# Kernel tuning notes

Measured on AMD Instinct MI355X. Metric: run time of the kernel, lower is better.

Reference implementation:

```python
import jax, jax.numpy as jnp
import numpy as np

# GNB per-element parameters [s, beta, R, C6] indexed by atomic number Z (rows not listed stay zero)
_ROWS = {
 1:[0.2772,1.7504,3.6516,95.99], 2:[0.2425,2.087,2.1843,40.67], 3:[0.3266,2.3073,1.2711,70.21],
 4:[0.3964,2.8811,3.3497,114.51], 5:[0.3121,2.6366,2.7079,152.36], 6:[0.2455,3.0189,1.8219,184.28],
 7:[0.2743,2.9432,2.4667,482.54], 8:[0.2577,2.7407,2.365,405.57], 9:[0.2791,2.5863,1.5062,218.45],
 10:[0.2378,2.5307,1.8233,174.81], 11:[0.2592,2.5679,1.3974,181.7], 12:[0.3837,2.9613,3.3515,263.02],
 13:[0.3013,3.2377,3.0102,228.1], 14:[0.3202,3.2749,3.1629,359.43], 15:[0.3399,3.7491,3.2554,3222.12],
 16:[0.3215,3.6718,2.9539,2144.49], 17:[0.3071,3.418,3.0368,2072.46], 18:[0.2752,3.3306,2.6598,1357.42],
 19:[0.2264,2.9736,4.0877,1406.65], 20:[0.4015,3.4464,4.1275,1058.36], 21:[0.9388,4.5955,9.7282,11498.73],
 22:[0.6048,3.5334,8.5322,3361.33], 23:[0.3678,3.068,7.2344,2095.91], 24:[0.2848,2.8393,5.3605,1049.31],
 25:[0.355,3.055,3.718,966.27], 26:[0.4406,3.2628,3.6408,1571.36], 27:[0.4124,3.2622,3.4961,1183.59],
 28:[0.3139,2.749,3.5108,787.76], 29:[0.3345,2.9097,3.0537,563.93], 30:[0.3391,2.9024,3.0261,592.91],
 31:[0.3146,3.3924,3.1735,430.82], 32:[0.3327,3.2804,3.1773,812.57], 33:[0.404,3.8757,3.8357,4533.53],
 34:[0.3343,3.8562,3.1109,3440.92], 35:[0.3242,3.7067,3.2122,3859.82], 36:[0.292,3.6457,2.8263,2729.6],
 37:[0.2677,3.4421,2.412,1864.19], 38:[0.3446,3.559,1.894,1175.73], 39:[1.0038,5.7293,11.2061,32141.18],
 40:[0.6146,5.075,6.821,27655.14], 41:[0.4244,3.7156,7.2367,2864.2], 42:[0.4882,3.6853,3.901,3563.45],
 43:[0.4439,3.6987,4.0857,3266.43], 44:[0.4736,3.7826,4.045,3967.23], 45:[0.4039,3.4706,3.4813,2233.82],
 46:[0.3188,3.3433,3.0487,1393.49], 47:[0.2948,3.1186,2.7795,1315.09], 48:[0.3012,3.0853,2.8673,1311.47],
 49:[0.3351,3.5452,3.3339,1460.56], 50:[0.3134,3.2997,3.0086,1662.99], 51:[0.4081,4.1277,3.9919,8089.97],
 52:[0.3585,4.1795,3.4209,6887.05], 53:[0.3574,4.0988,3.5649,8799.32], 54:[0.3134,4.0387,3.0288,6136.5],
 55:[0.2872,3.8468,2.262,3757.31], 56:[0.3788,4.0368,1.3837,2561.18], 57:[1.0851,6.1365,12.171,66580.83],
 72:[0.5577,5.213,6.0791,27593.76], 73:[0.5308,4.7637,5.7661,15364.65], 74:[0.3926,3.6018,3.6366,2734.5],
 75:[0.5351,3.9552,4.241,4801.82], 76:[0.4701,4.0278,4.1348,5685.94], 77:[0.3661,3.6123,3.4213,2786.0],
 78:[0.3411,3.6066,3.2486,2699.79], 79:[0.3164,3.3822,2.9588,2282.6], 80:[0.3047,3.375,2.9381,2476.79],
 81:[0.2802,3.3964,2.7711,2988.7], 82:[0.2682,3.2481,2.5816,2506.63], 83:[0.3876,4.1225,3.785,8916.84],
 84:[0.3679,4.2313,3.5381,8694.22], 85:[0.368,4.2455,3.6985,11821.61], 86:[0.3195,4.1784,3.0551,8410.64],
}
_TAB = np.zeros((87, 4), np.float32)
for _z, _v in _ROWS.items():
    _TAB[_z] = _v
GNB_TABLE = jnp.asarray(_TAB)
C_SP2 = jnp.asarray(np.array([0.2808, 3.0548, 2.2348, 429.69], np.float32))
C_SP3 = jnp.asarray(np.array([0.2455, 3.0189, 1.8219, 184.28], np.float32))
N_CN2 = jnp.asarray(np.array([0.2996, 3.02, 2.6454, 720.18], np.float32))
N_CN3 = jnp.asarray(np.array([0.2743, 2.9432, 2.4667, 482.54], np.float32))

BJ_A1, BJ_A2, BJ_ALPHA = 0.4, 4.0, 14.0
CUTOFF_LR, CUTOFF_START = 10.0, 8.0  # cutoff_start = cutoff_lr - 2.0


def _poly_envelope(x):
    # PolynomialCutoff.calculate_envelope with r_max=1, p=6:
    x6 = x ** 6
    env = 1.0 - 28.0 * x6 + 48.0 * x6 * x - 21.0 * x6 * x * x
    return env * (x < 1.0)


def _gnb_forward(lengths, Z, edge_index):
    n_nodes = Z.shape[0]
    sender, receiver = edge_index[0], edge_index[1]

    # coordination numbers via scatter-add on receiver
    cn = jnp.zeros((n_nodes,), jnp.int32).at[receiver].add(1)

    # species-indexed params with CN-adaptive selection for C and N
    params = GNB_TABLE[Z]  # [N, 4]
    c_params = jnp.where((cn <= 3)[:, None], C_SP2[None, :], C_SP3[None, :])
    n_params = jnp.where((cn <= 2)[:, None], N_CN2[None, :], N_CN3[None, :])
    params = jnp.where((Z == 6)[:, None], c_params, params)
    params = jnp.where((Z == 7)[:, None], n_params, params)

    R_i = params[:, 2]
    C6_i = params[:, 3]

    # geometric-mean combination rules per edge
    C6_ij = jnp.sqrt(C6_i[sender] * C6_i[receiver])
    R_ij = jnp.sqrt(R_i[sender] * R_i[receiver])

    r = lengths
    # BJ damping: f = 1 / (1 + 6 (r/r0)^(-alpha)), r0 = a1 sqrt(R_ij) + a2
    r0 = BJ_A1 * jnp.sqrt(R_ij) + BJ_A2
    f_damp = 1.0 / (1.0 + 6.0 * (r0 / r) ** BJ_ALPHA)

    e_edge = -C6_ij / (R_ij ** 6 + r ** 6) * f_damp

    # long-range polynomial cutoff switching from 1 at cutoff_start to 0 at cutoff_lr
    x = (r - CUTOFF_START) / (CUTOFF_LR - CUTOFF_START)
    env = jnp.where(r < CUTOFF_START, 1.0, _poly_envelope(x))
    e_edge = e_edge * env

    # scatter-sum to atoms; 0.5 to split symmetric pair energy over both directions
    node_energy = jnp.zeros((n_nodes,), e_edge.dtype).at[receiver].add(0.5 * e_edge)
    return node_energy


def setup_inputs() -> dict:
    key = jax.random.key(0)
    k1, k2, k3 = jax.random.split(key, 3)
    n_nodes, n_edges = 100000, 6400000
    Z = jax.random.randint(k1, (n_nodes,), 1, 87, dtype=jnp.int32)
    edge_index = jax.random.randint(k2, (2, n_edges), 0, n_nodes, dtype=jnp.int32)
    lengths = jax.random.uniform(k3, (n_edges,), jnp.float32, 1.0, 10.5)
    return {"Z": Z, "edge_index": edge_index, "lengths": lengths}


def reference(Z, edge_index, lengths):
    return _gnb_forward(lengths, Z, edge_index)
```

## Files before the change

### kernel.cpp

```cpp
#include <hip/hip_runtime.h>


#define B2SHIFT 10
#define B2SIZE  1024
#define TILE    4096
#define ESLICES 16
#define MAXB    128

__device__ __constant__ float2 GNB_RC6[87] = {
    {0.f, 0.f},
    {3.6516f, 95.99f},   {2.1843f, 40.67f},   {1.2711f, 70.21f},
    {3.3497f, 114.51f},  {2.7079f, 152.36f},  {1.8219f, 184.28f},
    {2.4667f, 482.54f},  {2.365f, 405.57f},   {1.5062f, 218.45f},
    {1.8233f, 174.81f},  {1.3974f, 181.7f},   {3.3515f, 263.02f},
    {3.0102f, 228.1f},   {3.1629f, 359.43f},  {3.2554f, 3222.12f},
    {2.9539f, 2144.49f}, {3.0368f, 2072.46f}, {2.6598f, 1357.42f},
    {4.0877f, 1406.65f}, {4.1275f, 1058.36f}, {9.7282f, 11498.73f},
    {8.5322f, 3361.33f}, {7.2344f, 2095.91f}, {5.3605f, 1049.31f},
    {3.718f, 966.27f},   {3.6408f, 1571.36f}, {3.4961f, 1183.59f},
    {3.5108f, 787.76f},  {3.0537f, 563.93f},  {3.0261f, 592.91f},
    {3.1735f, 430.82f},  {3.1773f, 812.57f},  {3.8357f, 4533.53f},
    {3.1109f, 3440.92f}, {3.2122f, 3859.82f}, {2.8263f, 2729.6f},
    {2.412f, 1864.19f},  {1.894f, 1175.73f},  {11.2061f, 32141.18f},
    {6.821f, 27655.14f}, {7.2367f, 2864.2f},  {3.901f, 3563.45f},
    {4.0857f, 3266.43f}, {4.045f, 3967.23f},  {3.4813f, 2233.82f},
    {3.0487f, 1393.49f}, {2.7795f, 1315.09f}, {2.8673f, 1311.47f},
    {3.3339f, 1460.56f}, {3.0086f, 1662.99f}, {3.9919f, 8089.97f},
    {3.4209f, 6887.05f}, {3.5649f, 8799.32f}, {3.0288f, 6136.5f},
    {2.262f, 3757.31f},  {1.3837f, 2561.18f}, {12.171f, 66580.83f},
    {0.f,0.f},{0.f,0.f},{0.f,0.f},{0.f,0.f},{0.f,0.f},{0.f,0.f},{0.f,0.f},
    {0.f,0.f},{0.f,0.f},{0.f,0.f},{0.f,0.f},{0.f,0.f},{0.f,0.f},{0.f,0.f},
    {6.0791f, 27593.76f}, {5.7661f, 15364.65f}, {3.6366f, 2734.5f},
    {4.241f, 4801.82f},   {4.1348f, 5685.94f},  {3.4213f, 2786.0f},
    {3.2486f, 2699.79f},  {2.9588f, 2282.6f},   {2.9381f, 2476.79f},
    {2.7711f, 2988.7f},   {2.5816f, 2506.63f},  {3.785f, 8916.84f},
    {3.5381f, 8694.22f},  {3.6985f, 11821.61f}, {3.0551f, 8410.64f},
};

__global__ void gnb_init(const int* __restrict__ Z, unsigned* __restrict__ isCN,
                         int nw, int n_nodes, int* __restrict__ zp, int zwords) {
    int stride = gridDim.x * blockDim.x;
    int t0 = blockIdx.x * blockDim.x + threadIdx.x;
    for (int i = t0; i < zwords; i += stride) zp[i] = 0;
    for (int w = t0; w < nw; w += stride) {
        unsigned m = 0;
        int base = w << 5;
        int lim = n_nodes - base; if (lim > 32) lim = 32;
        for (int k = 0; k < lim; ++k) {
            int z = Z[base + k];
            if (z == 6 || z == 7) m |= (1u << k);
        }
        isCN[w] = m;
    }
}

__global__ void __launch_bounds__(256)
gnb_scatter(const int* __restrict__ send, const int* __restrict__ recv,
            const float* __restrict__ len, const unsigned* __restrict__ isCN,
            int* __restrict__ cn,
            uint2* __restrict__ buckets, unsigned* __restrict__ cursor,
            uint4* __restrict__ ovrec, unsigned* __restrict__ ocur,
            int n_edges, int cap, unsigned ocap, int NB2) {
    __shared__ unsigned cnt[MAXB];
    __shared__ unsigned pos[MAXB];
    __shared__ unsigned startp[MAXB + 1];
    __shared__ unsigned gbase[MAXB];
    __shared__ uint2 srec[TILE];
    __shared__ unsigned char bmap[TILE];
    const int tid = threadIdx.x;
    const int e0  = blockIdx.x * TILE;

    for (int b = tid; b < MAXB; b += 256) { cnt[b] = 0; pos[b] = 0; }
    __syncthreads();

    #pragma unroll
    for (int k = 0; k < 4; ++k) {
        int base = e0 + (k * 256 + tid) * 4;
        if (base + 3 < n_edges) {
            int4 rv = *(const int4*)(recv + base);
            int rr[4] = {rv.x, rv.y, rv.z, rv.w};
            #pragma unroll
            for (int j = 0; j < 4; ++j) {
                unsigned r = (unsigned)rr[j];
                atomicAdd(&cnt[r >> B2SHIFT], 1u);
                if ((isCN[r >> 5] >> (r & 31)) & 1u) atomicAdd(&cn[r], 1);
            }
        } else {
            int lim = n_edges - base; if (lim > 4) lim = 4;
            for (int j = 0; j < lim; ++j) {
                unsigned r = (unsigned)recv[base + j];
                atomicAdd(&cnt[r >> B2SHIFT], 1u);
                if ((isCN[r >> 5] >> (r & 31)) & 1u) atomicAdd(&cn[r], 1);
            }
        }
    }
    __syncthreads();

    if (tid == 0) {
        unsigned acc = 0;
        for (int b = 0; b < NB2; ++b) { startp[b] = acc; acc += cnt[b]; }
        startp[NB2] = acc;
    }
    __syncthreads();
    if (tid < NB2) gbase[tid] = atomicAdd(&cursor[tid], cnt[tid]);
    __syncthreads();

    #pragma unroll
    for (int k = 0; k < 4; ++k) {
        int base = e0 + (k * 256 + tid) * 4;
        if (base + 3 < n_edges) {
            int4  sv = *(const int4*)(send + base);
            int4  rv = *(const int4*)(recv + base);
            uint4 lv = *(const uint4*)(len + base);
            int ss[4] = {sv.x, sv.y, sv.z, sv.w};
            int rr[4] = {rv.x, rv.y, rv.z, rv.w};
            unsigned ll[4] = {lv.x, lv.y, lv.z, lv.w};
            #pragma unroll
            for (int j = 0; j < 4; ++j) {
                unsigned r = (unsigned)rr[j];
                unsigned b = r >> B2SHIFT;
                unsigned slot = startp[b] + atomicAdd(&pos[b], 1u);
                srec[slot] = make_uint2((unsigned)ss[j] | ((r & (B2SIZE - 1)) << 17), ll[j]);
                bmap[slot] = (unsigned char)b;
            }
        } else {
            int lim = n_edges - base; if (lim > 4) lim = 4;
            for (int j = 0; j < lim; ++j) {
                unsigned r = (unsigned)recv[base + j];
                unsigned b = r >> B2SHIFT;
                unsigned slot = startp[b] + atomicAdd(&pos[b], 1u);
                srec[slot] = make_uint2((unsigned)send[base + j] | ((r & (B2SIZE - 1)) << 17),
                                        ((const unsigned*)len)[base + j]);
                bmap[slot] = (unsigned char)b;
            }
        }
    }
    __syncthreads();

    unsigned total = startp[NB2];
    for (unsigned i = tid; i < total; i += 256) {
        unsigned b = bmap[i];
        unsigned g = gbase[b] + (i - startp[b]);
        uint2 rec = srec[i];
        if (g < (unsigned)cap) {
            buckets[(size_t)b * cap + g] = rec;
        } else {
            unsigned o = atomicAdd(ocur, 1u);
            unsigned r = ((unsigned)b << B2SHIFT) | ((rec.x >> 17) & (B2SIZE - 1));
            if (o < ocap) ovrec[o] = make_uint4(r, rec.x & 0x1FFFFu, rec.y, 0u);
        }
    }
}

__global__ void gnb_params(const int* __restrict__ Z, const int* __restrict__ cn,
                           float2* __restrict__ P2, int n_nodes) {
    int i = blockIdx.x * blockDim.x + threadIdx.x;
    if (i >= n_nodes) return;
    int z = Z[i];
    float Rp, C6;
    if (z == 6) {
        if (cn[i] <= 3) { Rp = 2.2348f; C6 = 429.69f; }
        else            { Rp = 1.8219f; C6 = 184.28f; }
    } else if (z == 7) {
        if (cn[i] <= 2) { Rp = 2.6454f; C6 = 720.18f; }
        else            { Rp = 2.4667f; C6 = 482.54f; }
    } else {
        float2 rc = GNB_RC6[z];
        Rp = rc.x; C6 = rc.y;
    }
    P2[i] = make_float2(sqrtf(C6), sqrtf(sqrtf(Rp)));
}

__device__ __forceinline__ float gnb_energy_eval(float2 ps, float2 pr, float rlen) {
    float env;
    if (rlen < 8.0f) {
        env = 1.0f;
    } else {
        float x = (rlen - 8.0f) * 0.5f;
        float x2 = x * x;
        float x6 = x2 * x2 * x2;
        env = 1.0f - 28.0f * x6 + 48.0f * x6 * x - 21.0f * x6 * x2;
    }
    float sR  = ps.y * pr.y;
    float C6  = ps.x * pr.x;
    float Rij = sR * sR;
    float R3  = Rij * Rij * Rij;
    float R6  = R3 * R3;
    float r0  = 0.4f * sR + 4.0f;
    float t   = r0 / rlen;
    float t2 = t * t, t4 = t2 * t2, t8 = t4 * t4;
    float t14 = t8 * t4 * t2;
    float fd = 1.0f / (1.0f + 6.0f * t14);
    float rl2 = rlen * rlen;
    float r6 = rl2 * rl2 * rl2;
    return -0.5f * C6 / (R6 + r6) * fd * env;
}

__global__ void __launch_bounds__(256)
gnb_energy(const uint2* __restrict__ buckets, const unsigned* __restrict__ cursor,
           const float2* __restrict__ P2, float* __restrict__ rep,
           int cap, int n_nodes) {
    __shared__ float  acc[B2SIZE];
    __shared__ float2 p2loc[B2SIZE];
    const int b   = blockIdx.x / ESLICES;
    const int sl  = blockIdx.x % ESLICES;
    const int tid = threadIdx.x;

    for (int i = tid; i < B2SIZE; i += 256) {
        acc[i] = 0.0f;
        int node = (b << B2SHIFT) + i;
        p2loc[i] = (node < n_nodes) ? P2[node] : make_float2(0.f, 0.f);
    }
    __syncthreads();

    unsigned count = cursor[b];
    if (count > (unsigned)cap) count = (unsigned)cap;
    unsigned seg = (count + ESLICES - 1) / ESLICES;
    unsigned st  = (unsigned)sl * seg;
    unsigned en  = st + seg; if (en > count) en = count;

    const uint2* src = buckets + (size_t)b * cap;
    for (unsigned i = st + tid; i < en; i += 256) {
        uint2 rec = src[i];
        float rlen = __uint_as_float(rec.y);
        if (rlen >= 10.0f) continue;
        unsigned s    = rec.x & 0x1FFFFu;
        unsigned rlow = (rec.x >> 17) & (B2SIZE - 1);
        float e = gnb_energy_eval(P2[s], p2loc[rlow], rlen);
        atomicAdd(&acc[rlow], e);
    }
    __syncthreads();

    float* dst = rep + (size_t)blockIdx.x * B2SIZE;
    for (int i = tid; i < B2SIZE; i += 256) dst[i] = acc[i];
}

__global__ void gnb_ovf_energy(const uint4* __restrict__ ovrec, const unsigned* __restrict__ ocur,
                               const float2* __restrict__ P2, float* __restrict__ ovf,
                               unsigned ocap) {
    unsigned n = *ocur; if (n > ocap) n = ocap;
    int stride = gridDim.x * blockDim.x;
    for (unsigned i = blockIdx.x * blockDim.x + threadIdx.x; i < n; i += stride) {
        uint4 rec = ovrec[i];
        float rlen = __uint_as_float(rec.z);
        if (rlen >= 10.0f) continue;
        float e = gnb_energy_eval(P2[rec.y], P2[rec.x], rlen);
        atomicAdd(&ovf[rec.x], e);
    }
}

__global__ void gnb_reduce(const float* __restrict__ rep, const float* __restrict__ ovf,
                           float* __restrict__ out, int n_nodes) {
    int i = blockIdx.x * blockDim.x + threadIdx.x;
    if (i >= n_nodes) return;
    int b = i >> B2SHIFT;
    int j = i & (B2SIZE - 1);
    const float* src = rep + ((size_t)b * ESLICES) * B2SIZE + j;
    float sum = ovf[i];
    #pragma unroll
    for (int s = 0; s < ESLICES; ++s) sum += src[(size_t)s * B2SIZE];
    out[i] = sum;
}

extern "C" void kernel_launch(void* const* d_in, const int* in_sizes, int n_in,
                              void* d_out, int out_size, void* d_ws, size_t ws_size,
                              hipStream_t stream) {
    const int*   Z    = (const int*)d_in[0];
    const int*   eidx = (const int*)d_in[1];
    const float* len  = (const float*)d_in[2];
    float*       out  = (float*)d_out;

    const int n_nodes = in_sizes[0];
    const int n_edges = in_sizes[2];
    const int* send = eidx;
    const int* recv = eidx + n_edges;

    const int NB2 = (n_nodes + B2SIZE - 1) >> B2SHIFT;
    const int nw  = (n_nodes + 31) >> 5;
    const int nwp = (nw + 7) & ~7;

    char* ws = (char*)d_ws;
    unsigned* cursor = (unsigned*)ws;
    unsigned* ocur   = (unsigned*)(ws + MAXB * 4);
    int*      cn     = (int*)(ws + (MAXB + 8) * 4);
    float*    ovf    = (float*)(ws + ((size_t)n_nodes + MAXB + 8) * 4);
    float2*   P2     = (float2*)(ws + ((size_t)2 * n_nodes + MAXB + 8) * 4);
    unsigned* isCN   = (unsigned*)(ws + ((size_t)4 * n_nodes + MAXB + 8) * 4);
    float*    rep    = (float*)((char*)isCN + (size_t)nwp * 4);
    size_t rep_w     = (size_t)NB2 * ESLICES * B2SIZE;
    char*     tail   = (char*)rep + rep_w * 4;

    size_t fixed_words = (size_t)4 * n_nodes + MAXB + 8 + nwp + rep_w;
    size_t total_words = ws_size / 4;
    size_t avail = total_words > fixed_words ? total_words - fixed_words : 0;
    size_t ovw = avail / 32;
    unsigned ocap = (unsigned)(ovw / 4);
    long cap = (long)((avail - ovw) / (2 * (size_t)NB2));
    if (cap > n_edges) cap = n_edges;
    if (cap < 0) cap = 0;
    uint4* ovrec   = (uint4*)tail;
    uint2* buckets = (uint2*)(tail + (size_t)ocap * 16);

    const int B = 256;
    int node_blocks = (n_nodes + B - 1) / B;
    int scat_blocks = (n_edges + TILE - 1) / TILE;
    int zero_words  = 2 * n_nodes + MAXB + 8;

    gnb_init<<<256, B, 0, stream>>>(Z, isCN, nw, n_nodes, (int*)ws, zero_words);
    gnb_scatter<<<scat_blocks, B, 0, stream>>>(send, recv, len, isCN, cn, buckets,
                                               cursor, ovrec, ocur, n_edges,
                                               (int)cap, ocap, NB2);
    gnb_params<<<node_blocks, B, 0, stream>>>(Z, cn, P2, n_nodes);
    gnb_energy<<<NB2 * ESLICES, B, 0, stream>>>(buckets, cursor, P2, rep, (int)cap, n_nodes);
    gnb_ovf_energy<<<8, B, 0, stream>>>(ovrec, ocur, P2, ovf, ocap);
    gnb_reduce<<<node_blocks, B, 0, stream>>>(rep, ovf, out, n_nodes);
}
```

Measured before the change: 212.6 us.

## Filter out-of-cutoff edges during bucketing and widen scatter and energy parallelism

Edges at or beyond the 10.0 cutoff are now dropped during the bucket scatter, so they are never written to or read back from the bucket buffers. The cutoff test in the energy kernel is removed. The scatter kernel moves to 512-thread blocks with two iterations per thread. The energy kernel doubles its slices per bucket and splits its shared accumulators into two padded copies to reduce atomic contention. The costs are an extra length load in the counting pass, more partial-sum rows for the reduce kernel to read, and a possible mismatch if the reduce kernel still assumes the old slice count.

```diff
diff --git a/kernel.cpp b/kernel.cpp
--- a/kernel.cpp
+++ b/kernel.cpp
@@ -4,7 +4,8 @@
 #define B2SHIFT 10
 #define B2SIZE  1024
 #define TILE    4096
-#define ESLICES 16
+#define SBLK    512
+#define ESLICES 32
 #define MAXB    128
 
 __device__ __constant__ float2 GNB_RC6[87] = {
@@ -54,7 +55,7 @@
     }
 }
 
-__global__ void __launch_bounds__(256)
+__global__ void __launch_bounds__(SBLK)
 gnb_scatter(const int* __restrict__ send, const int* __restrict__ recv,
             const float* __restrict__ len, const unsigned* __restrict__ isCN,
             int* __restrict__ cn,
@@ -70,26 +71,28 @@
     const int tid = threadIdx.x;
     const int e0  = blockIdx.x * TILE;
 
-    for (int b = tid; b < MAXB; b += 256) { cnt[b] = 0; pos[b] = 0; }
+    for (int b = tid; b < MAXB; b += SBLK) { cnt[b] = 0; pos[b] = 0; }
     __syncthreads();
 
     #pragma unroll
-    for (int k = 0; k < 4; ++k) {
-        int base = e0 + (k * 256 + tid) * 4;
+    for (int k = 0; k < 2; ++k) {
+        int base = e0 + (k * SBLK + tid) * 4;
         if (base + 3 < n_edges) {
-            int4 rv = *(const int4*)(recv + base);
+            int4   rv = *(const int4*)(recv + base);
+            float4 lv = *(const float4*)(len + base);
             int rr[4] = {rv.x, rv.y, rv.z, rv.w};
+            float ll[4] = {lv.x, lv.y, lv.z, lv.w};
             #pragma unroll
             for (int j = 0; j < 4; ++j) {
                 unsigned r = (unsigned)rr[j];
-                atomicAdd(&cnt[r >> B2SHIFT], 1u);
+                if (ll[j] < 10.0f) atomicAdd(&cnt[r >> B2SHIFT], 1u);
                 if ((isCN[r >> 5] >> (r & 31)) & 1u) atomicAdd(&cn[r], 1);
             }
         } else {
-            int lim = n_edges - base; if (lim > 4) lim = 4;
+            int lim = n_edges - base; if (lim < 0) lim = 0; if (lim > 4) lim = 4;
             for (int j = 0; j < lim; ++j) {
                 unsigned r = (unsigned)recv[base + j];
-                atomicAdd(&cnt[r >> B2SHIFT], 1u);
+                if (len[base + j] < 10.0f) atomicAdd(&cnt[r >> B2SHIFT], 1u);
                 if ((isCN[r >> 5] >> (r & 31)) & 1u) atomicAdd(&cn[r], 1);
             }
         }
@@ -106,17 +109,18 @@
     __syncthreads();
 
     #pragma unroll
-    for (int k = 0; k < 4; ++k) {
-        int base = e0 + (k * 256 + tid) * 4;
+    for (int k = 0; k < 2; ++k) {
+        int base = e0 + (k * SBLK + tid) * 4;
         if (base + 3 < n_edges) {
-            int4  sv = *(const int4*)(send + base);
-            int4  rv = *(const int4*)(recv + base);
-            uint4 lv = *(const uint4*)(len + base);
+            int4   sv = *(const int4*)(send + base);
+            int4   rv = *(const int4*)(recv + base);
+            uint4  lv = *(const uint4*)(len + base);
             int ss[4] = {sv.x, sv.y, sv.z, sv.w};
             int rr[4] = {rv.x, rv.y, rv.z, rv.w};
             unsigned ll[4] = {lv.x, lv.y, lv.z, lv.w};
             #pragma unroll
             for (int j = 0; j < 4; ++j) {
+                if (__uint_as_float(ll[j]) >= 10.0f) continue;
                 unsigned r = (unsigned)rr[j];
                 unsigned b = r >> B2SHIFT;
                 unsigned slot = startp[b] + atomicAdd(&pos[b], 1u);
@@ -124,13 +128,15 @@
                 bmap[slot] = (unsigned char)b;
             }
         } else {
-            int lim = n_edges - base; if (lim > 4) lim = 4;
+            int lim = n_edges - base; if (lim < 0) lim = 0; if (lim > 4) lim = 4;
             for (int j = 0; j < lim; ++j) {
+                unsigned lbits = ((const unsigned*)len)[base + j];
+                if (__uint_as_float(lbits) >= 10.0f) continue;
                 unsigned r = (unsigned)recv[base + j];
                 unsigned b = r >> B2SHIFT;
                 unsigned slot = startp[b] + atomicAdd(&pos[b], 1u);
                 srec[slot] = make_uint2((unsigned)send[base + j] | ((r & (B2SIZE - 1)) << 17),
-                                        ((const unsigned*)len)[base + j]);
+                                        lbits);
                 bmap[slot] = (unsigned char)b;
             }
         }
@@ -138,7 +144,7 @@
     __syncthreads();
 
     unsigned total = startp[NB2];
-    for (unsigned i = tid; i < total; i += 256) {
+    for (unsigned i = tid; i < total; i += SBLK) {
         unsigned b = bmap[i];
         unsigned g = gbase[b] + (i - startp[b]);
         uint2 rec = srec[i];
@@ -200,14 +206,15 @@
 gnb_energy(const uint2* __restrict__ buckets, const unsigned* __restrict__ cursor,
            const float2* __restrict__ P2, float* __restrict__ rep,
            int cap, int n_nodes) {
-    __shared__ float  acc[B2SIZE];
+    __shared__ float  acc[2][B2SIZE + 8];
     __shared__ float2 p2loc[B2SIZE];
     const int b   = blockIdx.x / ESLICES;
     const int sl  = blockIdx.x % ESLICES;
     const int tid = threadIdx.x;
-
+    const int rr  = (tid >> 6) & 1;
+
+    for (int i = tid; i < 2 * (B2SIZE + 8); i += 256) acc[0][i] = 0.0f;
     for (int i = tid; i < B2SIZE; i += 256) {
-        acc[i] = 0.0f;
         int node = (b << B2SHIFT) + i;
         p2loc[i] = (node < n_nodes) ? P2[node] : make_float2(0.f, 0.f);
     }
@@ -222,17 +229,15 @@
     const uint2* src = buckets + (size_t)b * cap;
     for (unsigned i = st + tid; i < en; i += 256) {
         uint2 rec = src[i];
-        float rlen = __uint_as_float(rec.y);
-        if (rlen >= 10.0f) continue;
         unsigned s    = rec.x & 0x1FFFFu;
         unsigned rlow = (rec.x >> 17) & (B2SIZE - 1);
-        float e = gnb_energy_eval(P2[s], p2loc[rlow], rlen);
-        atomicAdd(&acc[rlow], e);
+        float e = gnb_energy_eval(P2[s], p2loc[rlow], __uint_as_float(rec.y));
+        atomicAdd(&acc[rr][rlow], e);
     }
     __syncthreads();
 
     float* dst = rep + (size_t)blockIdx.x * B2SIZE;
-    for (int i = tid; i < B2SIZE; i += 256) dst[i] = acc[i];
+    for (int i = tid; i < B2SIZE; i += 256) dst[i] = acc[0][i] + acc[1][i];
 }
 
 __global__ void gnb_ovf_energy(const uint4* __restrict__ ovrec, const unsigned* __restrict__ ocur,
@@ -307,9 +312,9 @@
     int zero_words  = 2 * n_nodes + MAXB + 8;
 
     gnb_init<<<256, B, 0, stream>>>(Z, isCN, nw, n_nodes, (int*)ws, zero_words);
-    gnb_scatter<<<scat_blocks, B, 0, stream>>>(send, recv, len, isCN, cn, buckets,
-                                               cursor, ovrec, ocur, n_edges,
-                                               (int)cap, ocap, NB2);
+    gnb_scatter<<<scat_blocks, SBLK, 0, stream>>>(send, recv, len, isCN, cn, buckets,
+                                                  cursor, ovrec, ocur, n_edges,
+                                                  (int)cap, ocap, NB2);
     gnb_params<<<node_blocks, B, 0, stream>>>(Z, cn, P2, n_nodes);
     gnb_energy<<<NB2 * ESLICES, B, 0, stream>>>(buckets, cursor, P2, rep, (int)cap, n_nodes);
     gnb_ovf_energy<<<8, B, 0, stream>>>(ovrec, ocur, P2, ovf, ocap);
```

New measurement: 203.2 us. -4.4%, faster.
